# Performance work log

Measured on AMD Instinct MI355X. Metric: run time of the kernel, lower is better.

## Reference

```python
import jax, jax.numpy as jnp
import numpy as np

BEV_H = 150; BEV_W = 150; D = 4; NCAM = 6; C = 128
FH = 48; FW = 88            # camera feature map size
IMG_H = 480.0; IMG_W = 800.0  # raw image size used to normalize uv
PC = np.array([-51.2, -51.2, -5.0, 51.2, 51.2, 3.0], np.float32)  # pc_range


def setup_inputs() -> dict:
    key = jax.random.key(0)
    # GenerateGrid buffer: (D, 3, h, w) with channels (x, y, z), normalized to [0,1]
    z = PC[5] - PC[2]
    zs = (np.linspace(0.5, z - 0.5, D) / z).astype(np.float32)
    xs = (np.linspace(0.5, BEV_W - 0.5, BEV_W) / BEV_W).astype(np.float32)
    ys = (np.linspace(0.5, BEV_H - 0.5, BEV_H) / BEV_H).astype(np.float32)
    g = np.zeros((D, 3, BEV_H, BEV_W), np.float32)
    g[:, 0] = xs[None, None, :]
    g[:, 1] = ys[None, :, None]
    g[:, 2] = zs[:, None, None]
    # realistic surround-camera rig: 6 cams looking outward every 60 deg
    I = np.zeros((1, NCAM, 3, 3), np.float32)
    E = np.zeros((1, NCAM, 4, 4), np.float32)
    for i in range(NCAM):
        I[0, i] = [[500.0, 0.0, 400.0], [0.0, 500.0, 240.0], [0.0, 0.0, 1.0]]
        yaw = 2.0 * np.pi * i / NCAM
        fwd = np.array([np.cos(yaw), np.sin(yaw), 0.0])
        right = np.array([np.sin(yaw), -np.cos(yaw), 0.0])
        down = np.array([0.0, 0.0, -1.0])
        R = np.stack([right, down, fwd])  # rows = camera axes in ego frame
        campos = np.array([1.5 * np.cos(yaw), 1.5 * np.sin(yaw), 1.5])
        E[0, i, :3, :3] = R
        E[0, i, :3, 3] = -R @ campos
        E[0, i, 3, 3] = 1.0
    feat = jax.random.normal(key, (1, NCAM, FH, FW, C), jnp.float32)
    return {"feat": feat, "I": jnp.asarray(I), "E": jnp.asarray(E), "grid_3d": jnp.asarray(g)}


def _forward(feat, I, E, grid_3d):
    b, n = I.shape[:2]
    d, _, h, w = grid_3d.shape
    Q = h * w
    scale = jnp.asarray([PC[3] - PC[0], PC[4] - PC[1], PC[5] - PC[2]], feat.dtype)
    off = jnp.asarray([PC[0], PC[1], PC[2]], feat.dtype)
    # (D, Q, 3) ego-frame 3D reference points, then homogeneous (D, Q, 4)
    rp = grid_3d.reshape(d, 3, Q).transpose(0, 2, 1) * scale + off
    rp4 = jnp.concatenate([rp, jnp.ones((d, Q, 1), rp.dtype)], axis=-1)
    # lidar2img = I @ E[:, :, :3, :] -> (b, n, 3, 4); project -> (b, n, D, Q, 3)
    l2i = jnp.einsum('bnij,bnjk->bnik', I, E[:, :, :3, :])
    proj = jnp.einsum('bnij,dqj->bndqi', l2i, rp4)
    eps = 1e-5
    zc = proj[..., 2]
    mask = zc > eps
    uv = proj[..., :2] / jnp.maximum(zc, eps)[..., None]
    u = uv[..., 0] / IMG_W
    v = uv[..., 1] / IMG_H
    mask = mask & (u > 0.0) & (u < 1.0) & (v > 0.0) & (v < 1.0)
    # bilinear grid_sample (align_corners=False, zero padding) at (u, v)
    px = u * FW - 0.5
    py = v * FH - 0.5
    x0 = jnp.floor(px)
    y0 = jnp.floor(py)
    wx1 = px - x0; wy1 = py - y0
    wx0 = 1.0 - wx1; wy0 = 1.0 - wy1
    x0i = x0.astype(jnp.int32)
    y0i = y0.astype(jnp.int32)
    ff = feat.reshape(b, n, FH * FW, C)

    def gather(xi, yi, wt):
        valid = (xi >= 0) & (xi < FW) & (yi >= 0) & (yi < FH)
        idx = (jnp.clip(yi, 0, FH - 1) * FW + jnp.clip(xi, 0, FW - 1)).reshape(b, n, d * Q)
        g = jnp.take_along_axis(ff, idx[..., None], axis=2).reshape(b, n, d, Q, C)
        return g * (wt * valid.astype(feat.dtype))[..., None]

    sampled = (gather(x0i, y0i, wx0 * wy0) + gather(x0i + 1, y0i, wx1 * wy0)
               + gather(x0i, y0i + 1, wx0 * wy1) + gather(x0i + 1, y0i + 1, wx1 * wy1))
    # mask-weighted fusion over cameras and pillar points (BEVFormer SCA)
    m = mask.astype(feat.dtype)
    out = jnp.einsum('bndq,bndqc->bqc', m, sampled)
    cnt = jnp.clip(m.sum(axis=(1, 2)), 1.0, None)
    return out / cnt[..., None]  # (b, Q, C)


def reference(feat, I, E, grid_3d):
    return _forward(feat, I, E, grid_3d)
```

## Files before the change

kernel.cpp:

```cpp
#include <hip/hip_runtime.h>

#define BEV_H 150
#define BEV_W 150
#define NCAM  6
#define CC    128
#define FH    48
#define FW    88
#define IMG_Hf 480.0f
#define IMG_Wf 800.0f
#define NPTS  24

__device__ __forceinline__ float rdlanef(float x, int l) {
    return __uint_as_float((unsigned)__builtin_amdgcn_readlane((int)__float_as_uint(x), l));
}

__global__ __launch_bounds__(128, 8) void bev_sample_kernel(
    const float* __restrict__ feat,
    const float* __restrict__ I_,
    const float* __restrict__ E_,
    const float* __restrict__ grid,
    float* __restrict__ out)
{
    const int tid  = threadIdx.x;
    const int lane = tid & 63;
    const int wv   = tid >> 6;
    const int l32  = lane & 31;
    const bool lowhalf = (lane < 32);

    const int r    = blockIdx.x & 7;
    const int i    = blockIdx.x >> 3;
    const int row0 = (r < 4) ? 0 : 38;
    const int nrow = (r < 4) ? 38 : 37;
    const int c3   = r & 3;
    const int col0 = c3 * 19;
    const int wr   = (c3 == 3) ? 18 : 19;
    if (i >= nrow * wr) return;
    int ph, pw;
    if (wr == 19) { ph = i / 19; pw = i - ph * 19; }
    else          { ph = i / 18; pw = i - ph * 18; }
    ph += row0; pw += col0;

    const int h  = ph * 2 + wv;
    const int wA = pw * 2;
    const int qA = h * BEV_W + wA;

    const bool actA = (lane < NPTS);
    const bool actB = (lane >= 32) && (lane < 32 + NPTS);
    float gx = 0.f, gy = 0.f, gz = 0.f;
    int n = 0;
    if (actA || actB) {
        n = l32 >> 2;
        const int d = l32 & 3;
        const int wc = wA + (actB ? 1 : 0);
        gx = grid[((d * 3 + 0) * BEV_H + h) * BEV_W + wc];
        gy = grid[((d * 3 + 1) * BEV_H + h) * BEV_W + wc];
        gz = grid[((d * 3 + 2) * BEV_H + h) * BEV_W + wc];
    }

    __shared__ __align__(16) float s_l2i[NCAM][12];
    if (tid < NCAM * 12) {
        const int nn = tid / 12, rr = tid % 12;
        const int ii = rr >> 2, j = rr & 3;
        float acc = 0.f;
        #pragma unroll
        for (int k = 0; k < 3; ++k)
            acc += I_[nn * 9 + ii * 3 + k] * E_[nn * 16 + k * 4 + j];
        s_l2i[nn][rr] = acc;
    }
    __syncthreads();

    int   iT = 0, iB = 0;
    float wTL = 0.f, wTR = 0.f, wBL = 0.f, wBR = 0.f;
    bool  m = false;

    if (actA || actB) {
        const float x = gx * 102.4f - 51.2f;
        const float y = gy * 102.4f - 51.2f;
        const float z = gz * 8.0f   - 5.0f;

        const float4 M0 = *(const float4*)&s_l2i[n][0];
        const float4 M1 = *(const float4*)&s_l2i[n][4];
        const float4 M2 = *(const float4*)&s_l2i[n][8];
        const float p0 = M0.x * x + M0.y * y + M0.z * z + M0.w;
        const float p1 = M1.x * x + M1.y * y + M1.z * z + M1.w;
        const float p2 = M2.x * x + M2.y * y + M2.z * z + M2.w;

        const float eps = 1e-5f;
        const float zc = fmaxf(p2, eps);
        const float u = (p0 / zc) * (1.0f / IMG_Wf);
        const float v = (p1 / zc) * (1.0f / IMG_Hf);
        m = (p2 > eps) && (u > 0.f) && (u < 1.f) && (v > 0.f) && (v < 1.f);

        const float px = u * (float)FW - 0.5f;
        const float py = v * (float)FH - 0.5f;
        const float fx0 = floorf(px), fy0 = floorf(py);
        const int x0 = (int)fx0, y0 = (int)fy0;
        const int x1 = x0 + 1,   y1 = y0 + 1;
        const float wx1 = px - fx0, wy1 = py - fy0;
        const float wx0 = 1.f - wx1, wy0 = 1.f - wy1;

        const bool vx0 = (x0 >= 0) && (x0 < FW);
        const bool vx1 = (x1 >= 0) && (x1 < FW);
        const bool vy0 = (y0 >= 0) && (y0 < FH);
        const bool vy1 = (y1 >= 0) && (y1 < FH);
        const int cx0 = min(max(x0, 0), FW - 1), cx1 = min(max(x1, 0), FW - 1);
        const int cy0 = min(max(y0, 0), FH - 1), cy1 = min(max(y1, 0), FH - 1);

        const float w0v = wx0 * wy0 * ((vx0 && vy0) ? 1.f : 0.f);
        const float w1v = wx1 * wy0 * ((vx1 && vy0) ? 1.f : 0.f);
        const float w2v = wx0 * wy1 * ((vx0 && vy1) ? 1.f : 0.f);
        const float w3v = wx1 * wy1 * ((vx1 && vy1) ? 1.f : 0.f);

        const int bx = min(max(x0, 0), FW - 2);
        wTL = ((cx0 == bx)     ? w0v : 0.f) + ((cx1 == bx)     ? w1v : 0.f);
        wTR = ((cx0 == bx + 1) ? w0v : 0.f) + ((cx1 == bx + 1) ? w1v : 0.f);
        wBL = ((cx0 == bx)     ? w2v : 0.f) + ((cx1 == bx)     ? w3v : 0.f);
        wBR = ((cx0 == bx + 1) ? w2v : 0.f) + ((cx1 == bx + 1) ? w3v : 0.f);

        const int base = n * FH * FW;
        iT = (base + cy0 * FW + bx) * CC;
        iB = (base + cy1 * FW + bx) * CC;
    }

    const unsigned long long bal = __ballot(m);
    unsigned balA = (unsigned)(bal & 0xFFFFFFull);
    unsigned balB = (unsigned)((bal >> 32) & 0xFFFFFFull);
    const float cntA = fmaxf((float)__popc(balA), 1.f);
    const float cntB = fmaxf((float)__popc(balB), 1.f);

    float aAx = 0.f, aAy = 0.f, aAz = 0.f, aAw = 0.f;
    float aBx = 0.f, aBy = 0.f, aBz = 0.f, aBw = 0.f;
    const int loff = 4 * lane;

    while (balA | balB) {
        int eA0 = 0, eA1 = 0, eB0 = 32, eB1 = 32;
        float sA0 = 0.f, sA1 = 0.f, sB0 = 0.f, sB1 = 0.f;
        if (balA) {
            eA0 = __builtin_ctz(balA); balA &= balA - 1; sA0 = 1.f;
            if (balA) { eA1 = __builtin_ctz(balA); balA &= balA - 1; sA1 = 1.f; }
            else eA1 = eA0;
        }
        if (balB) {
            eB0 = 32 + __builtin_ctz(balB); balB &= balB - 1; sB0 = 1.f;
            if (balB) { eB1 = 32 + __builtin_ctz(balB); balB &= balB - 1; sB1 = 1.f; }
            else eB1 = eB0;
        }

        const int jTA0 = __builtin_amdgcn_readlane(iT, eA0), jBA0 = __builtin_amdgcn_readlane(iB, eA0);
        const int jTA1 = __builtin_amdgcn_readlane(iT, eA1), jBA1 = __builtin_amdgcn_readlane(iB, eA1);
        const int jTB0 = __builtin_amdgcn_readlane(iT, eB0), jBB0 = __builtin_amdgcn_readlane(iB, eB0);
        const int jTB1 = __builtin_amdgcn_readlane(iT, eB1), jBB1 = __builtin_amdgcn_readlane(iB, eB1);

        const float4 fTA0 = *(const float4*)(feat + jTA0 + loff);
        const float4 fBA0 = *(const float4*)(feat + jBA0 + loff);
        const float4 fTA1 = *(const float4*)(feat + jTA1 + loff);
        const float4 fBA1 = *(const float4*)(feat + jBA1 + loff);
        const float4 fTB0 = *(const float4*)(feat + jTB0 + loff);
        const float4 fBB0 = *(const float4*)(feat + jBB0 + loff);
        const float4 fTB1 = *(const float4*)(feat + jTB1 + loff);
        const float4 fBB1 = *(const float4*)(feat + jBB1 + loff);

        const float wTA0 = sA0 * (lowhalf ? rdlanef(wTL, eA0) : rdlanef(wTR, eA0));
        const float wBA0 = sA0 * (lowhalf ? rdlanef(wBL, eA0) : rdlanef(wBR, eA0));
        const float wTA1 = sA1 * (lowhalf ? rdlanef(wTL, eA1) : rdlanef(wTR, eA1));
        const float wBA1 = sA1 * (lowhalf ? rdlanef(wBL, eA1) : rdlanef(wBR, eA1));
        const float wTB0 = sB0 * (lowhalf ? rdlanef(wTL, eB0) : rdlanef(wTR, eB0));
        const float wBB0 = sB0 * (lowhalf ? rdlanef(wBL, eB0) : rdlanef(wBR, eB0));
        const float wTB1 = sB1 * (lowhalf ? rdlanef(wTL, eB1) : rdlanef(wTR, eB1));
        const float wBB1 = sB1 * (lowhalf ? rdlanef(wBL, eB1) : rdlanef(wBR, eB1));

        aAx += wTA0 * fTA0.x + wBA0 * fBA0.x + wTA1 * fTA1.x + wBA1 * fBA1.x;
        aAy += wTA0 * fTA0.y + wBA0 * fBA0.y + wTA1 * fTA1.y + wBA1 * fBA1.y;
        aAz += wTA0 * fTA0.z + wBA0 * fBA0.z + wTA1 * fTA1.z + wBA1 * fBA1.z;
        aAw += wTA0 * fTA0.w + wBA0 * fBA0.w + wTA1 * fTA1.w + wBA1 * fBA1.w;
        aBx += wTB0 * fTB0.x + wBB0 * fBB0.x + wTB1 * fTB1.x + wBB1 * fBB1.x;
        aBy += wTB0 * fTB0.y + wBB0 * fBB0.y + wTB1 * fTB1.y + wBB1 * fBB1.y;
        aBz += wTB0 * fTB0.z + wBB0 * fBB0.z + wTB1 * fTB1.z + wBB1 * fBB1.z;
        aBw += wTB0 * fTB0.w + wBB0 * fBB0.w + wTB1 * fTB1.w + wBB1 * fBB1.w;
    }

    aAx += __shfl_xor(aAx, 32);  aAy += __shfl_xor(aAy, 32);
    aAz += __shfl_xor(aAz, 32);  aAw += __shfl_xor(aAw, 32);
    aBx += __shfl_xor(aBx, 32);  aBy += __shfl_xor(aBy, 32);
    aBz += __shfl_xor(aBz, 32);  aBw += __shfl_xor(aBw, 32);

    const float inv = lowhalf ? (1.f / cntA) : (1.f / cntB);
    const int   q   = lowhalf ? qA : (qA + 1);
    float4 o;
    o.x = (lowhalf ? aAx : aBx) * inv;
    o.y = (lowhalf ? aAy : aBy) * inv;
    o.z = (lowhalf ? aAz : aBz) * inv;
    o.w = (lowhalf ? aAw : aBw) * inv;
    *(float4*)(out + q * CC + 4 * l32) = o;
}

extern "C" void kernel_launch(void* const* d_in, const int* in_sizes, int n_in,
                              void* d_out, int out_size, void* d_ws, size_t ws_size,
                              hipStream_t stream) {
    const float* feat = (const float*)d_in[0];
    const float* I_   = (const float*)d_in[1];
    const float* E_   = (const float*)d_in[2];
    const float* grid = (const float*)d_in[3];
    float* out        = (float*)d_out;

    bev_sample_kernel<<<8 * 722, 128, 0, stream>>>(feat, I_, E_, grid, out);
}
```

Measured before the change: 18.47 us.

## Split projection into separate kernel writing packed per-point sample records

Moves camera projection and bilinear weight computation into a new pre-pass kernel that writes a packed int4 record (two row indices plus fp16-packed weights) per point into workspace. The sampling kernel then reads one record per lane instead of computing grid loads, the l2i matrix and the projection, which removes the shared-memory sync and that ALU work. In exchange it adds a second launch and a round trip through global memory (about 8.6 MB written and read), and the weights are stored in fp16, which loses precision.

```diff
diff --git a/kernel.cpp b/kernel.cpp
--- a/kernel.cpp
+++ b/kernel.cpp
@@ -1,4 +1,5 @@
 #include <hip/hip_runtime.h>
+#include <hip/hip_fp16.h>
 
 #define BEV_H 150
 #define BEV_W 150
@@ -9,16 +10,100 @@
 #define IMG_Hf 480.0f
 #define IMG_Wf 800.0f
 #define NPTS  24
+#define QTOT  (BEV_H * BEV_W)
+#define GTOT  (QTOT * NPTS)
 
 __device__ __forceinline__ float rdlanef(float x, int l) {
     return __uint_as_float((unsigned)__builtin_amdgcn_readlane((int)__float_as_uint(x), l));
 }
 
-__global__ __launch_bounds__(128, 8) void bev_sample_kernel(
-    const float* __restrict__ feat,
+__global__ __launch_bounds__(256) void proj_kernel(
     const float* __restrict__ I_,
     const float* __restrict__ E_,
     const float* __restrict__ grid,
+    int4* __restrict__ rec)
+{
+    const int g = blockIdx.x * 256 + threadIdx.x;
+    if (g >= GTOT) return;
+    const int p = g / QTOT;
+    const int q = g - p * QTOT;
+    const int n = p >> 2;
+    const int d = p & 3;
+
+    float M[12];
+    #pragma unroll
+    for (int i = 0; i < 3; ++i) {
+        #pragma unroll
+        for (int j = 0; j < 4; ++j) {
+            float acc = 0.f;
+            #pragma unroll
+            for (int k = 0; k < 3; ++k)
+                acc += I_[n * 9 + i * 3 + k] * E_[n * 16 + k * 4 + j];
+            M[i * 4 + j] = acc;
+        }
+    }
+
+    const float gx = grid[(d * 3 + 0) * QTOT + q];
+    const float gy = grid[(d * 3 + 1) * QTOT + q];
+    const float gz = grid[(d * 3 + 2) * QTOT + q];
+    const float x = gx * 102.4f - 51.2f;
+    const float y = gy * 102.4f - 51.2f;
+    const float z = gz * 8.0f   - 5.0f;
+
+    const float p0 = M[0] * x + M[1] * y + M[2]  * z + M[3];
+    const float p1 = M[4] * x + M[5] * y + M[6]  * z + M[7];
+    const float p2 = M[8] * x + M[9] * y + M[10] * z + M[11];
+
+    const float eps = 1e-5f;
+    const float zc = fmaxf(p2, eps);
+    const float u = (p0 / zc) * (1.0f / IMG_Wf);
+    const float v = (p1 / zc) * (1.0f / IMG_Hf);
+    const bool m = (p2 > eps) && (u > 0.f) && (u < 1.f) && (v > 0.f) && (v < 1.f);
+
+    int4 o;
+    if (m) {
+        const float px = u * (float)FW - 0.5f;
+        const float py = v * (float)FH - 0.5f;
+        const float fx0 = floorf(px), fy0 = floorf(py);
+        const int x0 = (int)fx0, y0 = (int)fy0;
+        const int x1 = x0 + 1,   y1 = y0 + 1;
+        const float wx1 = px - fx0, wy1 = py - fy0;
+        const float wx0 = 1.f - wx1, wy0 = 1.f - wy1;
+
+        const bool vx0 = (x0 >= 0) && (x0 < FW);
+        const bool vx1 = (x1 >= 0) && (x1 < FW);
+        const bool vy0 = (y0 >= 0) && (y0 < FH);
+        const bool vy1 = (y1 >= 0) && (y1 < FH);
+        const int cx0 = min(max(x0, 0), FW - 1), cx1 = min(max(x1, 0), FW - 1);
+        const int cy0 = min(max(y0, 0), FH - 1), cy1 = min(max(y1, 0), FH - 1);
+
+        const float w0v = wx0 * wy0 * ((vx0 && vy0) ? 1.f : 0.f);
+        const float w1v = wx1 * wy0 * ((vx1 && vy0) ? 1.f : 0.f);
+        const float w2v = wx0 * wy1 * ((vx0 && vy1) ? 1.f : 0.f);
+        const float w3v = wx1 * wy1 * ((vx1 && vy1) ? 1.f : 0.f);
+
+        const int bx = min(max(x0, 0), FW - 2);
+        const float wTL = ((cx0 == bx)     ? w0v : 0.f) + ((cx1 == bx)     ? w1v : 0.f);
+        const float wTR = ((cx0 == bx + 1) ? w0v : 0.f) + ((cx1 == bx + 1) ? w1v : 0.f);
+        const float wBL = ((cx0 == bx)     ? w2v : 0.f) + ((cx1 == bx)     ? w3v : 0.f);
+        const float wBR = ((cx0 == bx + 1) ? w2v : 0.f) + ((cx1 == bx + 1) ? w3v : 0.f);
+
+        const int base = n * FH * FW;
+        o.x = (base + cy0 * FW + bx) * CC;
+        o.y = (base + cy1 * FW + bx) * CC;
+        __half2 hT = __floats2half2_rn(wTL, wTR);
+        __half2 hB = __floats2half2_rn(wBL, wBR);
+        o.z = *(int*)&hT;
+        o.w = *(int*)&hB;
+    } else {
+        o.x = -1; o.y = 0; o.z = 0; o.w = 0;
+    }
+    rec[g] = o;
+}
+
+__global__ __launch_bounds__(128, 8) void bev_sample_kernel(
+    const int4* __restrict__ rec,
+    const float* __restrict__ feat,
     float* __restrict__ out)
 {
     const int tid  = threadIdx.x;
@@ -46,83 +131,19 @@
 
     const bool actA = (lane < NPTS);
     const bool actB = (lane >= 32) && (lane < 32 + NPTS);
-    float gx = 0.f, gy = 0.f, gz = 0.f;
-    int n = 0;
+    bool valid = false;
+    int iT = 0, iB = 0;
+    unsigned wTu = 0, wBu = 0;
     if (actA || actB) {
-        n = l32 >> 2;
-        const int d = l32 & 3;
-        const int wc = wA + (actB ? 1 : 0);
-        gx = grid[((d * 3 + 0) * BEV_H + h) * BEV_W + wc];
-        gy = grid[((d * 3 + 1) * BEV_H + h) * BEV_W + wc];
-        gz = grid[((d * 3 + 2) * BEV_H + h) * BEV_W + wc];
-    }
-
-    __shared__ __align__(16) float s_l2i[NCAM][12];
-    if (tid < NCAM * 12) {
-        const int nn = tid / 12, rr = tid % 12;
-        const int ii = rr >> 2, j = rr & 3;
-        float acc = 0.f;
-        #pragma unroll
-        for (int k = 0; k < 3; ++k)
-            acc += I_[nn * 9 + ii * 3 + k] * E_[nn * 16 + k * 4 + j];
-        s_l2i[nn][rr] = acc;
-    }
-    __syncthreads();
-
-    int   iT = 0, iB = 0;
-    float wTL = 0.f, wTR = 0.f, wBL = 0.f, wBR = 0.f;
-    bool  m = false;
-
-    if (actA || actB) {
-        const float x = gx * 102.4f - 51.2f;
-        const float y = gy * 102.4f - 51.2f;
-        const float z = gz * 8.0f   - 5.0f;
-
-        const float4 M0 = *(const float4*)&s_l2i[n][0];
-        const float4 M1 = *(const float4*)&s_l2i[n][4];
-        const float4 M2 = *(const float4*)&s_l2i[n][8];
-        const float p0 = M0.x * x + M0.y * y + M0.z * z + M0.w;
-        const float p1 = M1.x * x + M1.y * y + M1.z * z + M1.w;
-        const float p2 = M2.x * x + M2.y * y + M2.z * z + M2.w;
-
-        const float eps = 1e-5f;
-        const float zc = fmaxf(p2, eps);
-        const float u = (p0 / zc) * (1.0f / IMG_Wf);
-        const float v = (p1 / zc) * (1.0f / IMG_Hf);
-        m = (p2 > eps) && (u > 0.f) && (u < 1.f) && (v > 0.f) && (v < 1.f);
-
-        const float px = u * (float)FW - 0.5f;
-        const float py = v * (float)FH - 0.5f;
-        const float fx0 = floorf(px), fy0 = floorf(py);
-        const int x0 = (int)fx0, y0 = (int)fy0;
-        const int x1 = x0 + 1,   y1 = y0 + 1;
-        const float wx1 = px - fx0, wy1 = py - fy0;
-        const float wx0 = 1.f - wx1, wy0 = 1.f - wy1;
-
-        const bool vx0 = (x0 >= 0) && (x0 < FW);
-        const bool vx1 = (x1 >= 0) && (x1 < FW);
-        const bool vy0 = (y0 >= 0) && (y0 < FH);
-        const bool vy1 = (y1 >= 0) && (y1 < FH);
-        const int cx0 = min(max(x0, 0), FW - 1), cx1 = min(max(x1, 0), FW - 1);
-        const int cy0 = min(max(y0, 0), FH - 1), cy1 = min(max(y1, 0), FH - 1);
-
-        const float w0v = wx0 * wy0 * ((vx0 && vy0) ? 1.f : 0.f);
-        const float w1v = wx1 * wy0 * ((vx1 && vy0) ? 1.f : 0.f);
-        const float w2v = wx0 * wy1 * ((vx0 && vy1) ? 1.f : 0.f);
-        const float w3v = wx1 * wy1 * ((vx1 && vy1) ? 1.f : 0.f);
-
-        const int bx = min(max(x0, 0), FW - 2);
-        wTL = ((cx0 == bx)     ? w0v : 0.f) + ((cx1 == bx)     ? w1v : 0.f);
-        wTR = ((cx0 == bx + 1) ? w0v : 0.f) + ((cx1 == bx + 1) ? w1v : 0.f);
-        wBL = ((cx0 == bx)     ? w2v : 0.f) + ((cx1 == bx)     ? w3v : 0.f);
-        wBR = ((cx0 == bx + 1) ? w2v : 0.f) + ((cx1 == bx + 1) ? w3v : 0.f);
-
-        const int base = n * FH * FW;
-        iT = (base + cy0 * FW + bx) * CC;
-        iB = (base + cy1 * FW + bx) * CC;
-    }
-
-    const unsigned long long bal = __ballot(m);
+        const int q = actB ? (qA + 1) : qA;
+        const int4 rv = rec[l32 * QTOT + q];
+        valid = (rv.x >= 0);
+        iT = valid ? rv.x : 0;
+        iB = rv.y;
+        wTu = (unsigned)rv.z; wBu = (unsigned)rv.w;
+    }
+
+    const unsigned long long bal = __ballot(valid);
     unsigned balA = (unsigned)(bal & 0xFFFFFFull);
     unsigned balB = (unsigned)((bal >> 32) & 0xFFFFFFull);
     const float cntA = fmaxf((float)__popc(balA), 1.f);
@@ -131,6 +152,9 @@
     float aAx = 0.f, aAy = 0.f, aAz = 0.f, aAw = 0.f;
     float aBx = 0.f, aBy = 0.f, aBz = 0.f, aBw = 0.f;
     const int loff = 4 * lane;
+
+    #define WSEL(uw) (lowhalf ? __half2float(__low2half(*(const __half2*)&(uw))) \
+                              : __half2float(__high2half(*(const __half2*)&(uw))))
 
     while (balA | balB) {
         int eA0 = 0, eA1 = 0, eB0 = 32, eB1 = 32;
@@ -160,14 +184,19 @@
         const float4 fTB1 = *(const float4*)(feat + jTB1 + loff);
         const float4 fBB1 = *(const float4*)(feat + jBB1 + loff);
 
-        const float wTA0 = sA0 * (lowhalf ? rdlanef(wTL, eA0) : rdlanef(wTR, eA0));
-        const float wBA0 = sA0 * (lowhalf ? rdlanef(wBL, eA0) : rdlanef(wBR, eA0));
-        const float wTA1 = sA1 * (lowhalf ? rdlanef(wTL, eA1) : rdlanef(wTR, eA1));
-        const float wBA1 = sA1 * (lowhalf ? rdlanef(wBL, eA1) : rdlanef(wBR, eA1));
-        const float wTB0 = sB0 * (lowhalf ? rdlanef(wTL, eB0) : rdlanef(wTR, eB0));
-        const float wBB0 = sB0 * (lowhalf ? rdlanef(wBL, eB0) : rdlanef(wBR, eB0));
-        const float wTB1 = sB1 * (lowhalf ? rdlanef(wTL, eB1) : rdlanef(wTR, eB1));
-        const float wBB1 = sB1 * (lowhalf ? rdlanef(wBL, eB1) : rdlanef(wBR, eB1));
+        const unsigned uTA0 = (unsigned)__builtin_amdgcn_readlane((int)wTu, eA0);
+        const unsigned uBA0 = (unsigned)__builtin_amdgcn_readlane((int)wBu, eA0);
+        const unsigned uTA1 = (unsigned)__builtin_amdgcn_readlane((int)wTu, eA1);
+        const unsigned uBA1 = (unsigned)__builtin_amdgcn_readlane((int)wBu, eA1);
+        const unsigned uTB0 = (unsigned)__builtin_amdgcn_readlane((int)wTu, eB0);
+        const unsigned uBB0 = (unsigned)__builtin_amdgcn_readlane((int)wBu, eB0);
+        const unsigned uTB1 = (unsigned)__builtin_amdgcn_readlane((int)wTu, eB1);
+        const unsigned uBB1 = (unsigned)__builtin_amdgcn_readlane((int)wBu, eB1);
+
+        const float wTA0 = sA0 * WSEL(uTA0), wBA0 = sA0 * WSEL(uBA0);
+        const float wTA1 = sA1 * WSEL(uTA1), wBA1 = sA1 * WSEL(uBA1);
+        const float wTB0 = sB0 * WSEL(uTB0), wBB0 = sB0 * WSEL(uBB0);
+        const float wTB1 = sB1 * WSEL(uTB1), wBB1 = sB1 * WSEL(uBB1);
 
         aAx += wTA0 * fTA0.x + wBA0 * fBA0.x + wTA1 * fTA1.x + wBA1 * fBA1.x;
         aAy += wTA0 * fTA0.y + wBA0 * fBA0.y + wTA1 * fTA1.y + wBA1 * fBA1.y;
@@ -178,6 +207,7 @@
         aBz += wTB0 * fTB0.z + wBB0 * fBB0.z + wTB1 * fTB1.z + wBB1 * fBB1.z;
         aBw += wTB0 * fTB0.w + wBB0 * fBB0.w + wTB1 * fTB1.w + wBB1 * fBB1.w;
     }
+    #undef WSEL
 
     aAx += __shfl_xor(aAx, 32);  aAy += __shfl_xor(aAy, 32);
     aAz += __shfl_xor(aAz, 32);  aAw += __shfl_xor(aAw, 32);
@@ -203,5 +233,7 @@
     const float* grid = (const float*)d_in[3];
     float* out        = (float*)d_out;
 
-    bev_sample_kernel<<<8 * 722, 128, 0, stream>>>(feat, I_, E_, grid, out);
-}
+    int4* rec = (int4*)d_ws;
+    proj_kernel<<<(GTOT + 255) / 256, 256, 0, stream>>>(I_, E_, grid, rec);
+    bev_sample_kernel<<<8 * 722, 128, 0, stream>>>(rec, feat, out);
+}
```

Result: slower. 24.73 us (+33.9%).
